# Kernel tuning notes

Measured on AMD Instinct MI355X. Metric: run time of the kernel, lower is better.

The kernel has to match this reference:

```python
import jax, jax.numpy as jnp
import numpy as np

DIM = 1024
N_HEADS = 16
HEAD_DIM = DIM // N_HEADS


def setup_inputs() -> dict:
    key = jax.random.key(0)
    ks = jax.random.split(key, 7)
    s = 1.0 / np.sqrt(DIM)
    return {
        "hidden_states": jax.random.normal(ks[0], (1, 4096, DIM), dtype=jnp.float32),
        "Wq": jax.random.uniform(ks[1], (DIM, DIM), jnp.float32, -s, s),
        "bq": jax.random.uniform(ks[2], (DIM,), jnp.float32, -s, s),
        "Wk": jax.random.uniform(ks[3], (DIM, DIM), jnp.float32, -s, s),
        "bk": jax.random.uniform(ks[4], (DIM,), jnp.float32, -s, s),
        "Wv": jax.random.uniform(ks[5], (DIM, DIM), jnp.float32, -s, s),
        "bv": jax.random.uniform(ks[6], (DIM,), jnp.float32, -s, s),
    }


def _split_heads(x):
    # [B, S, DIM] -> [B, H, S, HEAD_DIM]
    b, s, _ = x.shape
    return x.reshape(b, s, N_HEADS, HEAD_DIM).transpose(0, 2, 1, 3)


def reference(hidden_states, Wq, bq, Wk, bk, Wv, bv):
    q = _split_heads(hidden_states @ Wq + bq)
    k = _split_heads(hidden_states @ Wk + bk)
    v = _split_heads(hidden_states @ Wv + bv)
    scores = jnp.einsum("bhqd,bhkd->bhqk", q, k) / np.sqrt(HEAD_DIM).astype(np.float32)
    probs = jax.nn.softmax(scores, axis=-1)  # dropout prob = 0 -> identity
    ctx = jnp.einsum("bhqk,bhkd->bhqd", probs, v)
    b, h, s, d = ctx.shape
    return ctx.transpose(0, 2, 1, 3).reshape(b, s, h * d)
```

## Files before the change

kernel.cpp:

```cpp
#include <hip/hip_runtime.h>
#include <hip/hip_bf16.h>

#define S_LEN 4096
#define DIM   1024
#define NH    16
#define HD    64

typedef unsigned short u16;
typedef short  bf16x8 __attribute__((ext_vector_type(8)));
typedef float  f32x4  __attribute__((ext_vector_type(4)));

__device__ __forceinline__ u16 f2bf(float f){
  union { float f; unsigned u; } x; x.f = f;
  unsigned u = x.u;
  return (u16)((u + 0x7FFFu + ((u >> 16) & 1u)) >> 16);
}
__device__ __forceinline__ unsigned pk2(float a, float b){
  union { __hip_bfloat162 h; unsigned u; } x;
  x.h = __float22bfloat162_rn(float2{a, b});
  return x.u;
}
__device__ __forceinline__ void ld2lds16(const u16* g, u16* l){
  __builtin_amdgcn_global_load_lds((const __attribute__((address_space(1))) void*)g,
                                   (__attribute__((address_space(3))) void*)l, 16, 0, 0);
}

__global__ __launch_bounds__(256) void fill_sentinel(float* __restrict__ out, int n){
  int i = blockIdx.x * 256 + threadIdx.x;
  if (i < n) out[i] = 77.0f;
}

__global__ __launch_bounds__(256) void conv_x(const float* __restrict__ X, u16* __restrict__ Xb){
  size_t i = ((size_t)blockIdx.x * 256 + threadIdx.x) * 8;
  float4 v0 = *(const float4*)(X + i);
  float4 v1 = *(const float4*)(X + i + 4);
  uint4 w;
  w.x = pk2(v0.x, v0.y); w.y = pk2(v0.z, v0.w);
  w.z = pk2(v1.x, v1.y); w.w = pk2(v1.z, v1.w);
  *(uint4*)(Xb + i) = w;
}

__global__ __launch_bounds__(256) void transpose_w(
    const float* __restrict__ W0, const float* __restrict__ W1, const float* __restrict__ W2,
    u16* __restrict__ Wt)
{
  const float* W = blockIdx.z==0 ? W0 : blockIdx.z==1 ? W1 : W2;
  u16* T = Wt + (size_t)blockIdx.z * DIM * DIM;
  __shared__ __align__(16) u16 tile[64*72];
  int k0 = blockIdx.x*64, n0 = blockIdx.y*64;
  int t = threadIdx.x;
  #pragma unroll
  for (int i = 0; i < 4; ++i){
    int idx = t + i*256;
    int row = idx >> 4, col4 = (idx & 15) * 4;
    float4 v = *(const float4*)(W + (size_t)(k0+row)*DIM + n0 + col4);
    tile[(col4+0)*72 + row] = f2bf(v.x);
    tile[(col4+1)*72 + row] = f2bf(v.y);
    tile[(col4+2)*72 + row] = f2bf(v.z);
    tile[(col4+3)*72 + row] = f2bf(v.w);
  }
  __syncthreads();
  #pragma unroll
  for (int i = 0; i < 2; ++i){
    int idx = t + i*256;
    int n = idx >> 3, k16 = (idx & 7) * 8;
    *(int4*)(T + (size_t)(n0+n)*DIM + k0 + k16) = *(const int4*)(tile + n*72 + k16);
  }
}

__device__ __forceinline__ void qkv_epilogue(
    int z, int m0, int n0, int wm, int wn, int quad, int l15,
    const f32x4 acc[4][4], const float* bias,
    u16* __restrict__ qb, u16* __restrict__ kf_out, u16* __restrict__ vf_out)
{
  #pragma unroll
  for (int nt=0; nt<4; ++nt){
    int n = n0 + wn + nt*16 + l15;
    float bv = bias[n];
    int h = n >> 6, d = n & 63;
    #pragma unroll
    for (int mt=0; mt<4; ++mt){
      int mb = m0 + wm + mt*16 + quad*4;
      f32x4 c = acc[mt][nt];
      if (z == 0){
        #pragma unroll
        for (int r=0; r<4; ++r)
          qb[(size_t)(mb + r)*DIM + n] = f2bf((c[r] + bv) * 0.125f);
      } else if (z == 1){
        int half = d >> 5, quadk = (d >> 3) & 3, j = d & 7;
        #pragma unroll
        for (int r=0; r<4; ++r){
          int s = mb + r;
          size_t idx = ((((size_t)h*256 + (s >> 4))*2 + half)*64 + quadk*16 + (s & 15))*8 + j;
          kf_out[idx] = f2bf(c[r] + bv);
        }
      } else {
        int kt64 = mb >> 6, c2 = (mb >> 5) & 1, quadv = (mb >> 3) & 3, j0 = mb & 7;
        int dt = d >> 4, l15v = d & 15;
        size_t base = (((((size_t)h*64 + kt64)*4 + dt)*2 + c2)*64 + quadv*16 + l15v)*8 + j0;
        ushort4 p;
        p.x = f2bf(c[0]+bv); p.y = f2bf(c[1]+bv);
        p.z = f2bf(c[2]+bv); p.w = f2bf(c[3]+bv);
        *(ushort4*)(vf_out + base) = p;
      }
    }
  }
}

__global__ __launch_bounds__(256) void qkv_gemm_fast(
    const u16* __restrict__ Xbf, const u16* __restrict__ Wt,
    const float* __restrict__ b0, const float* __restrict__ b1, const float* __restrict__ b2,
    u16* __restrict__ qb, u16* __restrict__ kf_out, u16* __restrict__ vf_out)
{
  int z = blockIdx.z;
  const u16* Wz = Wt + (size_t)z * DIM * DIM;
  const float* bias = z==0 ? b0 : z==1 ? b1 : b2;

  __shared__ __align__(16) u16 As[128*32];
  __shared__ __align__(16) u16 Bs[128*32];

  int m0 = blockIdx.x * 128, n0 = blockIdx.y * 128;
  int t = threadIdx.x, wave = t >> 6, lane = t & 63, quad = lane >> 4, l15 = lane & 15;
  int wm = (wave >> 1) * 64, wn = (wave & 1) * 64;

  f32x4 acc[4][4];
  #pragma unroll
  for (int i=0;i<4;++i)
    #pragma unroll
    for (int j=0;j<4;++j) acc[i][j] = (f32x4){0.f,0.f,0.f,0.f};

  int srow = wave*32 + (lane >> 2);
  int skc  = (lane & 3) * 8;
  const u16* gA0 = Xbf + (size_t)(m0 + srow)*DIM + skc;
  const u16* gA1 = gA0 + (size_t)16*DIM;
  const u16* gB0 = Wz  + (size_t)(n0 + srow)*DIM + skc;
  const u16* gB1 = gB0 + (size_t)16*DIM;
  u16* lA0 = As + srow*32 + skc;
  u16* lA1 = lA0 + 16*32;
  u16* lB0 = Bs + srow*32 + skc;
  u16* lB1 = lB0 + 16*32;

  for (int kt = 0; kt < 32; ++kt){
    int ko = kt * 32;
    __syncthreads();
    ld2lds16(gA0 + ko, lA0);
    ld2lds16(gA1 + ko, lA1);
    ld2lds16(gB0 + ko, lB0);
    ld2lds16(gB1 + ko, lB1);
    __syncthreads();
    bf16x8 af[4], bfr[4];
    #pragma unroll
    for (int mt=0; mt<4; ++mt) af[mt]  = *(const bf16x8*)(As + (wm + mt*16 + l15)*32 + quad*8);
    #pragma unroll
    for (int nt=0; nt<4; ++nt) bfr[nt] = *(const bf16x8*)(Bs + (wn + nt*16 + l15)*32 + quad*8);
    #pragma unroll
    for (int mt=0; mt<4; ++mt)
      #pragma unroll
      for (int nt=0; nt<4; ++nt)
        acc[mt][nt] = __builtin_amdgcn_mfma_f32_16x16x32_bf16(af[mt], bfr[nt], acc[mt][nt], 0, 0, 0);
  }
  qkv_epilogue(z, m0, n0, wm, wn, quad, l15, acc, bias, qb, kf_out, vf_out);
}

__global__ __launch_bounds__(256) void qkv_gemm_legacy(
    const float* __restrict__ X,
    const float* __restrict__ Wq, const float* __restrict__ Wk, const float* __restrict__ Wv,
    const float* __restrict__ b0, const float* __restrict__ b1, const float* __restrict__ b2,
    u16* __restrict__ qb, u16* __restrict__ kf_out, u16* __restrict__ vf_out)
{
  int z = blockIdx.z;
  const float* W    = z==0 ? Wq : z==1 ? Wk : Wv;
  const float* bias = z==0 ? b0 : z==1 ? b1 : b2;

  __shared__ __align__(16) u16 As[128*40];
  __shared__ __align__(16) u16 Bs[128*40];

  int m0 = blockIdx.x * 128, n0 = blockIdx.y * 128;
  int t = threadIdx.x, wave = t >> 6, lane = t & 63, quad = lane >> 4, l15 = lane & 15;
  int wm = (wave >> 1) * 64, wn = (wave & 1) * 64;

  f32x4 acc[4][4];
  #pragma unroll
  for (int i=0;i<4;++i)
    #pragma unroll
    for (int j=0;j<4;++j) acc[i][j] = (f32x4){0.f,0.f,0.f,0.f};

  int sr = t >> 2, sc = (t & 3) * 8;
  const float* gA0 = X + (size_t)(m0 + sr) * DIM + sc;
  const float* gA1 = X + (size_t)(m0 + 64 + sr) * DIM + sc;
  int br = t >> 3, bc = (t & 7) * 16;
  const float* gW = W + (size_t)br * DIM + n0 + bc;

  for (int kt = 0; kt < 32; ++kt){
    int ko = kt * 32;
    float4 a00 = *(const float4*)(gA0 + ko);
    float4 a01 = *(const float4*)(gA0 + ko + 4);
    float4 a10 = *(const float4*)(gA1 + ko);
    float4 a11 = *(const float4*)(gA1 + ko + 4);
    float4 w0  = *(const float4*)(gW + (size_t)ko*DIM);
    float4 w1  = *(const float4*)(gW + (size_t)ko*DIM + 4);
    float4 w2  = *(const float4*)(gW + (size_t)ko*DIM + 8);
    float4 w3  = *(const float4*)(gW + (size_t)ko*DIM + 12);
    int4 pa0, pa1;
    pa0.x = pk2(a00.x,a00.y); pa0.y = pk2(a00.z,a00.w);
    pa0.z = pk2(a01.x,a01.y); pa0.w = pk2(a01.z,a01.w);
    pa1.x = pk2(a10.x,a10.y); pa1.y = pk2(a10.z,a10.w);
    pa1.z = pk2(a11.x,a11.y); pa1.w = pk2(a11.z,a11.w);
    u16 wb[16];
    wb[0]=f2bf(w0.x); wb[1]=f2bf(w0.y); wb[2]=f2bf(w0.z); wb[3]=f2bf(w0.w);
    wb[4]=f2bf(w1.x); wb[5]=f2bf(w1.y); wb[6]=f2bf(w1.z); wb[7]=f2bf(w1.w);
    wb[8]=f2bf(w2.x); wb[9]=f2bf(w2.y); wb[10]=f2bf(w2.z); wb[11]=f2bf(w2.w);
    wb[12]=f2bf(w3.x); wb[13]=f2bf(w3.y); wb[14]=f2bf(w3.z); wb[15]=f2bf(w3.w);
    __syncthreads();
    *(int4*)(As + sr*40 + sc)      = pa0;
    *(int4*)(As + (64+sr)*40 + sc) = pa1;
    #pragma unroll
    for (int j=0;j<16;++j) Bs[(bc+j)*40 + br] = wb[j];
    __syncthreads();
    bf16x8 af[4], bfr[4];
    #pragma unroll
    for (int mt=0; mt<4; ++mt) af[mt]  = *(const bf16x8*)(As + (wm + mt*16 + l15)*40 + quad*8);
    #pragma unroll
    for (int nt=0; nt<4; ++nt) bfr[nt] = *(const bf16x8*)(Bs + (wn + nt*16 + l15)*40 + quad*8);
    #pragma unroll
    for (int mt=0; mt<4; ++mt)
      #pragma unroll
      for (int nt=0; nt<4; ++nt)
        acc[mt][nt] = __builtin_amdgcn_mfma_f32_16x16x32_bf16(af[mt], bfr[nt], acc[mt][nt], 0, 0, 0);
  }
  qkv_epilogue(z, m0, n0, wm, wn, quad, l15, acc, bias, qb, kf_out, vf_out);
}

#define PSTR 72
__global__ __launch_bounds__(256, 2) void attn(
    const u16* __restrict__ Qb, const u16* __restrict__ Kf,
    const u16* __restrict__ Vf, float* __restrict__ out)
{
  int h = blockIdx.y;
  int t = threadIdx.x, wave = t >> 6, lane = t & 63, quad = lane >> 4, l15 = lane & 15;
  int q0 = blockIdx.x * 128 + wave * 32;

  __shared__ __align__(16) u16 Ps[4*16*PSTR];
  u16* Pw = Ps + wave * (16*PSTR);

  const u16* Kfh = Kf + (size_t)h * 256*2*64*8;
  const u16* Vfh = Vf + (size_t)h * 64*4*2*64*8;

  bf16x8 qf[2][2];
  #pragma unroll
  for (int qs=0; qs<2; ++qs){
    const u16* Qp = Qb + (size_t)(q0 + qs*16 + l15)*DIM + h*HD;
    qf[qs][0] = *(const bf16x8*)(Qp + quad*8);
    qf[qs][1] = *(const bf16x8*)(Qp + 32 + quad*8);
  }

  f32x4 O[2][4];
  #pragma unroll
  for (int qs=0; qs<2; ++qs)
    #pragma unroll
    for (int dt=0; dt<4; ++dt) O[qs][dt] = (f32x4){0.f,0.f,0.f,0.f};
  float lsum[2] = {0.f, 0.f};

  for (int kt = 0; kt < 64; ++kt){
    bf16x8 kfr[4][2];
    #pragma unroll
    for (int kn=0; kn<4; ++kn)
      #pragma unroll
      for (int hf=0; hf<2; ++hf)
        kfr[kn][hf] = *(const bf16x8*)(Kfh + ((((size_t)kt*4 + kn)*2 + hf)*64 + lane)*8);
    bf16x8 vfr[4][2];
    #pragma unroll
    for (int dt=0; dt<4; ++dt)
      #pragma unroll
      for (int c2=0; c2<2; ++c2)
        vfr[dt][c2] = *(const bf16x8*)(Vfh + ((((size_t)kt*4 + dt)*2 + c2)*64 + lane)*8);

    #pragma unroll
    for (int qs=0; qs<2; ++qs){
      f32x4 st[4];
      #pragma unroll
      for (int kn=0; kn<4; ++kn){
        f32x4 zz = (f32x4){0.f,0.f,0.f,0.f};
        zz = __builtin_amdgcn_mfma_f32_16x16x32_bf16(kfr[kn][0], qf[qs][0], zz, 0,0,0);
        zz = __builtin_amdgcn_mfma_f32_16x16x32_bf16(kfr[kn][1], qf[qs][1], zz, 0,0,0);
        st[kn] = zz;
      }
      float ls = 0.f;
      #pragma unroll
      for (int kn=0; kn<4; ++kn)
        #pragma unroll
        for (int r=0; r<4; ++r){
          float p = __expf(st[kn][r]);
          st[kn][r] = p;
          ls += p;
        }
      lsum[qs] += ls;
      __builtin_amdgcn_wave_barrier();
      #pragma unroll
      for (int kn=0; kn<4; ++kn){
        uint2 w;
        w.x = pk2(st[kn][0], st[kn][1]);
        w.y = pk2(st[kn][2], st[kn][3]);
        *(uint2*)(Pw + l15*PSTR + kn*16 + quad*4) = w;
      }
      __builtin_amdgcn_wave_barrier();
      bf16x8 pf0 = *(const bf16x8*)(Pw + l15*PSTR + quad*8);
      bf16x8 pf1 = *(const bf16x8*)(Pw + l15*PSTR + 32 + quad*8);
      __builtin_amdgcn_wave_barrier();
      #pragma unroll
      for (int dt=0; dt<4; ++dt){
        f32x4 o = O[qs][dt];
        o = __builtin_amdgcn_mfma_f32_16x16x32_bf16(vfr[dt][0], pf0, o, 0,0,0);
        o = __builtin_amdgcn_mfma_f32_16x16x32_bf16(vfr[dt][1], pf1, o, 0,0,0);
        O[qs][dt] = o;
      }
    }
  }
  #pragma unroll
  for (int qs=0; qs<2; ++qs){
    float l = lsum[qs];
    l += __shfl_xor(l, 16, 64);
    l += __shfl_xor(l, 32, 64);
    float inv = 1.0f / l;
    int query = q0 + qs*16 + l15;
    #pragma unroll
    for (int dt=0; dt<4; ++dt){
      float4 v;
      v.x = O[qs][dt][0]*inv; v.y = O[qs][dt][1]*inv;
      v.z = O[qs][dt][2]*inv; v.w = O[qs][dt][3]*inv;
      *(float4*)(out + (size_t)query*DIM + h*HD + dt*16 + quad*4) = v;
    }
  }
}

extern "C" void kernel_launch(void* const* d_in, const int* in_sizes, int n_in,
                              void* d_out, int out_size, void* d_ws, size_t ws_size,
                              hipStream_t stream)
{
  const float* X  = (const float*)d_in[0];
  const float* Wq = (const float*)d_in[1];
  const float* bq = (const float*)d_in[2];
  const float* Wk = (const float*)d_in[3];
  const float* bk = (const float*)d_in[4];
  const float* Wv = (const float*)d_in[5];
  const float* bv = (const float*)d_in[6];
  float* out = (float*)d_out;
  u16*   ws  = (u16*)d_ws;

  const size_t SD = (size_t)S_LEN * DIM;
  const size_t need_fast = (4*SD + 3*(size_t)DIM*DIM) * sizeof(u16);
  const size_t need_min  = (size_t)24 * 1024 * 1024;

  if (ws_size >= need_fast){
    u16* xbf = ws;
    u16* wt  = xbf + SD;
    u16* qb  = wt + 3*(size_t)DIM*DIM;
    u16* kf  = qb + SD;
    u16* vf  = kf + SD;
    conv_x       <<<dim3((int)(SD/8/256)), 256, 0, stream>>>(X, xbf);
    transpose_w  <<<dim3(16,16,3), 256, 0, stream>>>(Wq, Wk, Wv, wt);
    qkv_gemm_fast<<<dim3(32, 8, 3), 256, 0, stream>>>(xbf, wt, bq, bk, bv, qb, kf, vf);
    attn         <<<dim3(32, 16   ), 256, 0, stream>>>(qb, kf, vf, out);
  } else if (ws_size >= need_min){
    u16* qb = ws;
    u16* kf = qb + SD;
    u16* vf = kf + SD;
    qkv_gemm_legacy<<<dim3(32, 8, 3), 256, 0, stream>>>(X, Wq, Wk, Wv, bq, bk, bv, qb, kf, vf);
    attn           <<<dim3(32, 16   ), 256, 0, stream>>>(qb, kf, vf, out);
  } else {
    fill_sentinel<<<(out_size + 255)/256, 256, 0, stream>>>(out, out_size);
  }
}
```

Measured before the change: 221.2 us.

## Double-buffer K/V tiles in LDS, use exp2 with folded scale, MFMA row sums

The attention kernel now stages each K/V tile into a double-buffered LDS region with async global-to-LDS loads, so the next tile is prefetched while the current one is computed. All four waves share a single copy of each tile instead of each wave loading it from global memory separately. The Q scale now folds in log2(e), so the softmax uses exp2f in place of __expf. Row sums are accumulated with an extra MFMA against a ones vector in place of scalar adds and shuffles. The trade-offs are two more MFMAs per step, a block-wide barrier every iteration, and dropping the min-2-blocks launch bound, which may change occupancy.

After: 260.3 us. 17.7% more time.

```diff
diff --git a/kernel.cpp b/kernel.cpp
--- a/kernel.cpp
+++ b/kernel.cpp
@@ -24,6 +24,8 @@
   __builtin_amdgcn_global_load_lds((const __attribute__((address_space(1))) void*)g,
                                    (__attribute__((address_space(3))) void*)l, 16, 0, 0);
 }
+
+#define QSCALE 0.1803368801111204f
 
 __global__ __launch_bounds__(256) void fill_sentinel(float* __restrict__ out, int n){
   int i = blockIdx.x * 256 + threadIdx.x;
@@ -85,7 +87,7 @@
       if (z == 0){
         #pragma unroll
         for (int r=0; r<4; ++r)
-          qb[(size_t)(mb + r)*DIM + n] = f2bf((c[r] + bv) * 0.125f);
+          qb[(size_t)(mb + r)*DIM + n] = f2bf((c[r] + bv) * QSCALE);
       } else if (z == 1){
         int half = d >> 5, quadk = (d >> 3) & 3, j = d & 7;
         #pragma unroll
@@ -232,7 +234,7 @@
 }
 
 #define PSTR 72
-__global__ __launch_bounds__(256, 2) void attn(
+__global__ __launch_bounds__(256) void attn(
     const u16* __restrict__ Qb, const u16* __restrict__ Kf,
     const u16* __restrict__ Vf, float* __restrict__ out)
 {
@@ -240,11 +242,15 @@
   int t = threadIdx.x, wave = t >> 6, lane = t & 63, quad = lane >> 4, l15 = lane & 15;
   int q0 = blockIdx.x * 128 + wave * 32;
 
+  __shared__ __align__(16) u16 KV[2][16*512];
   __shared__ __align__(16) u16 Ps[4*16*PSTR];
   u16* Pw = Ps + wave * (16*PSTR);
 
-  const u16* Kfh = Kf + (size_t)h * 256*2*64*8;
-  const u16* Vfh = Vf + (size_t)h * 64*4*2*64*8;
+  const u16* Kfh = Kf + (size_t)h * 262144;
+  const u16* Vfh = Vf + (size_t)h * 262144;
+
+  short ov = (l15 == 0) ? (short)0x3F80 : (short)0;
+  bf16x8 a_one = (bf16x8){ov,ov,ov,ov,ov,ov,ov,ov};
 
   bf16x8 qf[2][2];
   #pragma unroll
@@ -259,21 +265,39 @@
   for (int qs=0; qs<2; ++qs)
     #pragma unroll
     for (int dt=0; dt<4; ++dt) O[qs][dt] = (f32x4){0.f,0.f,0.f,0.f};
-  float lsum[2] = {0.f, 0.f};
+  f32x4 lacc[2] = {(f32x4){0.f,0.f,0.f,0.f}, (f32x4){0.f,0.f,0.f,0.f}};
+
+  #define STAGE(kt_, buf_)                                                         \
+    {                                                                              \
+      int kt8 = (kt_) * 8;                                                         \
+      _Pragma("unroll")                                                            \
+      for (int c = 0; c < 4; ++c){                                                 \
+        int g = wave + c*4;                                                        \
+        const u16* src = (g < 8) ? (Kfh + (size_t)(kt8 + g)*512 + lane*8)          \
+                                 : (Vfh + (size_t)(kt8 + g - 8)*512 + lane*8);     \
+        ld2lds16(src, &KV[buf_][g*512 + lane*8]);                                  \
+      }                                                                            \
+    }
+
+  STAGE(0, 0);
+  __syncthreads();
 
   for (int kt = 0; kt < 64; ++kt){
-    bf16x8 kfr[4][2];
+    int buf = kt & 1;
+    if (kt + 1 < 64) STAGE(kt + 1, buf ^ 1);
+
+    const u16* kvb = KV[buf];
+    bf16x8 kfr[4][2], vfr[4][2];
     #pragma unroll
     for (int kn=0; kn<4; ++kn)
       #pragma unroll
       for (int hf=0; hf<2; ++hf)
-        kfr[kn][hf] = *(const bf16x8*)(Kfh + ((((size_t)kt*4 + kn)*2 + hf)*64 + lane)*8);
-    bf16x8 vfr[4][2];
+        kfr[kn][hf] = *(const bf16x8*)(kvb + (kn*2 + hf)*512 + lane*8);
     #pragma unroll
     for (int dt=0; dt<4; ++dt)
       #pragma unroll
       for (int c2=0; c2<2; ++c2)
-        vfr[dt][c2] = *(const bf16x8*)(Vfh + ((((size_t)kt*4 + dt)*2 + c2)*64 + lane)*8);
+        vfr[dt][c2] = *(const bf16x8*)(kvb + (8 + dt*2 + c2)*512 + lane*8);
 
     #pragma unroll
     for (int qs=0; qs<2; ++qs){
@@ -285,16 +309,11 @@
         zz = __builtin_amdgcn_mfma_f32_16x16x32_bf16(kfr[kn][1], qf[qs][1], zz, 0,0,0);
         st[kn] = zz;
       }
-      float ls = 0.f;
       #pragma unroll
       for (int kn=0; kn<4; ++kn)
         #pragma unroll
-        for (int r=0; r<4; ++r){
-          float p = __expf(st[kn][r]);
-          st[kn][r] = p;
-          ls += p;
-        }
-      lsum[qs] += ls;
+        for (int r=0; r<4; ++r)
+          st[kn][r] = exp2f(st[kn][r]);
       __builtin_amdgcn_wave_barrier();
       #pragma unroll
       for (int kn=0; kn<4; ++kn){
@@ -307,6 +326,8 @@
       bf16x8 pf0 = *(const bf16x8*)(Pw + l15*PSTR + quad*8);
       bf16x8 pf1 = *(const bf16x8*)(Pw + l15*PSTR + 32 + quad*8);
       __builtin_amdgcn_wave_barrier();
+      lacc[qs] = __builtin_amdgcn_mfma_f32_16x16x32_bf16(a_one, pf0, lacc[qs], 0,0,0);
+      lacc[qs] = __builtin_amdgcn_mfma_f32_16x16x32_bf16(a_one, pf1, lacc[qs], 0,0,0);
       #pragma unroll
       for (int dt=0; dt<4; ++dt){
         f32x4 o = O[qs][dt];
@@ -315,12 +336,12 @@
         O[qs][dt] = o;
       }
     }
-  }
+    __syncthreads();
+  }
+
   #pragma unroll
   for (int qs=0; qs<2; ++qs){
-    float l = lsum[qs];
-    l += __shfl_xor(l, 16, 64);
-    l += __shfl_xor(l, 32, 64);
+    float l = __shfl(lacc[qs][0], l15, 64);
     float inv = 1.0f / l;
     int query = q0 + qs*16 + l15;
     #pragma unroll
```
